# Kernel tuning notes

Measured on AMD Instinct MI355X. Metric: run time of the kernel, lower is better.

## Reference

```python
import jax, jax.numpy as jnp
import numpy as np

N = 100_000   # nodes
E = 6_400_000 # edges
R = 90        # relations
NB = 3        # num_blocks


def setup_inputs() -> dict:
    key = jax.random.key(0)
    ks = jax.random.split(key, 10)
    x = jax.random.normal(ks[0], (N, 3), jnp.float32)
    edge_index = jax.random.randint(ks[1], (2, E), 0, N, dtype=jnp.int32)
    edge_type = jax.random.randint(ks[2], (E,), 0, R, dtype=jnp.int32)
    batch = jnp.zeros((N,), jnp.int32)  # single graph, as in source
    p = lambda k, shape: (jax.random.normal(k, shape, jnp.float32) * 0.1)
    # block-diagonal weights: [R, NB, in_b, out_b]
    W1, root1, b1 = p(ks[3], (R, NB, 1, 2)), p(ks[4], (3, 6)), jnp.zeros((6,), jnp.float32)
    W2, root2, b2 = p(ks[5], (R, NB, 2, 1)), p(ks[6], (6, 3)), jnp.zeros((3,), jnp.float32)
    W3, root3, b3 = p(ks[7], (R, NB, 1, 2)), p(ks[8], (3, 6)), jnp.zeros((6,), jnp.float32)
    return dict(x=x, edge_index=edge_index, batch=batch, edge_type=edge_type,
                W1=W1, root1=root1, b1=b1, W2=W2, root2=root2, b2=b2,
                W3=W3, root3=root3, b3=b3)


def _rgcn(x, src, dst, edge_type, W, root, bias, aggr):
    # block-diagonal per-relation transform of gathered source features
    nb, in_b, out_b = W.shape[1], W.shape[2], W.shape[3]
    xb = x[src].reshape(-1, nb, in_b)                      # [E, NB, in_b]
    msg = jnp.einsum('ebi,ebio->ebo', xb, W[edge_type])    # [E, NB, out_b]
    msg = msg.reshape(-1, nb * out_b)                      # [E, out]
    if aggr == 'mean':
        # per-(dst node, relation) normalization, as in FastRGCNConv
        comb = dst * R + edge_type                         # [E]
        cnt = jax.ops.segment_sum(jnp.ones((msg.shape[0],), msg.dtype), comb,
                                  num_segments=N * R)      # [N*R]
        msg = msg / jnp.clip(cnt[comb], 1.0)[:, None]
    agg = jax.ops.segment_sum(msg, dst, num_segments=N)    # [N, out]
    return agg + x @ root + bias


def reference(x, edge_index, batch, edge_type, W1, root1, b1, W2, root2, b2, W3, root3, b3):
    src, dst = edge_index[0], edge_index[1]
    h = jax.nn.relu(_rgcn(x, src, dst, edge_type, W1, root1, b1, 'mean'))
    # dropout is identity in eval mode
    h = jax.nn.relu(_rgcn(h, src, dst, edge_type, W2, root2, b2, 'add'))
    h = jax.nn.relu(_rgcn(h, src, dst, edge_type, W3, root3, b3, 'mean'))
    # global mean pool over batch (single graph here, kept general)
    num_graphs = 1
    s = jax.ops.segment_sum(h, batch, num_segments=num_graphs)
    c = jax.ops.segment_sum(jnp.ones((h.shape[0],), h.dtype), batch, num_segments=num_graphs)
    pooled = s / jnp.clip(c, 1.0)[:, None]
    return jax.nn.log_softmax(pooled, axis=1)
```

## Files before the change

### kernel.cpp

```cpp
#include <hip/hip_runtime.h>


#define NREL   90
#define BSH    7
#define BNODES 128
#define NBINS  1024
#define NB2    784
#define GCH    8704
#define KPT    17
#define SPK    11056
#define CAPB   10496
#define NV4    6
#define STAGE  9088
#define LPD    16
#define SENT   0xFFFFFFFFu

__device__ __forceinline__ float frelu(float v) { return v > 0.0f ? v : 0.0f; }

__launch_bounds__(512)
__global__ void group_k(const float* __restrict__ x, float4* __restrict__ x4,
                        int N, int gNp,
                        const int* __restrict__ src, const int* __restrict__ dst,
                        const int* __restrict__ et, int* __restrict__ gcount,
                        unsigned* __restrict__ regions, int E) {
    int tid = threadIdx.x;
    if (blockIdx.x < gNp) {
        int i = blockIdx.x * 512 + tid;
        if (i < N) x4[i] = make_float4(x[3 * i], x[3 * i + 1], x[3 * i + 2], 0.0f);
        return;
    }
    __shared__ int s_cur[NB2];
    __shared__ int s_pend[NB2];
    __shared__ int s_off[NB2];
    __shared__ unsigned s_pack[SPK];
    int chunk = blockIdx.x - gNp;
    int e0 = chunk * GCH;
    int cnt = min(GCH, E - e0);
    for (int i = tid; i < NB2; i += 512) s_pend[i] = 0;
    __syncthreads();
    unsigned rec[KPT];
    int bkt[KPT];
#pragma unroll
    for (int k = 0; k < KPT; k++) {
        int q = tid + k * 512;
        if (q < cnt) {
            int e = e0 + q;
            int d = dst[e];
            bkt[k] = d >> BSH;
            rec[k] = (unsigned)src[e] | ((unsigned)et[e] << 17) |
                     ((unsigned)(d & (BNODES - 1)) << 24);
            atomicAdd(&s_pend[bkt[k]], 1);
        } else bkt[k] = -1;
    }
    __syncthreads();
    if (tid < 49) {
        int loc[16];
        int s = 0;
        int b0 = tid * 16;
#pragma unroll
        for (int k = 0; k < 16; k++) {
            int plen = (s_pend[b0 + k] + 3) & ~3;
            loc[k] = plen; s += plen;
        }
        int inc = s;
#pragma unroll
        for (int off = 1; off < 64; off <<= 1) {
            int u = __shfl_up(inc, off);
            if (tid >= off) inc += u;
        }
        int run = inc - s;
#pragma unroll
        for (int k = 0; k < 16; k++) {
            s_cur[b0 + k] = run;
            run += loc[k];
            s_pend[b0 + k] = run;
        }
    }
    __syncthreads();
    int T = s_pend[NB2 - 1];
    for (int b = tid; b < NB2; b += 512) {
        int st = s_cur[b];
        int plen = s_pend[b] - st;
        if (plen > 0) {
            int gb = atomicAdd(&gcount[b], plen);
            if (gb + plen <= CAPB) {
                s_off[b] = gb - st;
            } else {
                s_off[b] = 0x40000000;
                unsigned* reg = regions + (size_t)b * CAPB;
                for (int j = min(gb, CAPB); j < CAPB; j++) reg[j] = SENT;
            }
        } else s_off[b] = 0x40000000;
    }
    for (int i = tid; i < T; i += 512) s_pack[i] = SENT;
    __syncthreads();
#pragma unroll
    for (int k = 0; k < KPT; k++) {
        if (bkt[k] >= 0) {
            int p = atomicAdd(&s_cur[bkt[k]], 1);
            s_pack[p] = rec[k];
        }
    }
    __syncthreads();
    int nv = T >> 2;
    for (int i4 = tid; i4 < nv; i4 += 512) {
        int i = i4 << 2;
        int lo = 0, hi = NB2 - 1;
        while (lo < hi) {
            int mid = (lo + hi) >> 1;
            if (s_pend[mid] > i) hi = mid; else lo = mid + 1;
        }
        int loc = s_off[lo] + i;
        if (loc < CAPB) {
            uint4 v = make_uint4(s_pack[i], s_pack[i + 1],
                                 s_pack[i + 2], s_pack[i + 3]);
            *(uint4*)(regions + (size_t)lo * CAPB + loc) = v;
        }
    }
}

__launch_bounds__(512)
__global__ void sortb_l1_k(const int* __restrict__ gcount, unsigned* regions,
                           int2* __restrict__ rowseg,
                           const float4* __restrict__ x4, const float* __restrict__ W,
                           const float* __restrict__ root, const float* __restrict__ bias,
                           float4* __restrict__ h1p, int N) {
    __shared__ unsigned stage32[STAGE];
    __shared__ unsigned hist8w[BNODES * 90 / 4];
    __shared__ int hh[BNODES], cur[BNODES], base_[BNODES];
    __shared__ float4 w4[NREL * 2];
    int tid = threadIdx.x, b = blockIdx.x;
    for (int i = tid; i < BNODES * 90 / 4; i += 512) hist8w[i] = 0u;
    for (int i = tid; i < NREL * 2; i += 512) {
        int r = i >> 1;
        w4[i] = (i & 1) ? make_float4(W[r * 6 + 4], W[r * 6 + 5], 0.f, 0.f)
                        : make_float4(W[r * 6], W[r * 6 + 1], W[r * 6 + 2], W[r * 6 + 3]);
    }
    __syncthreads();
    int fill = gcount[b];
    if (fill > CAPB) fill = CAPB;
    const uint4* reg4 = (const uint4*)(regions + (size_t)b * CAPB);
    int nv = fill >> 2;
    uint4 rec4[NV4];
#define HIST1(P) if ((P) != SENT) { \
        unsigned bi_ = ((P) >> 24) * 90u + (((P) >> 17) & 127u); \
        atomicAdd(&hist8w[bi_ >> 2], 1u << ((bi_ & 3) << 3)); }
#pragma unroll
    for (int k = 0; k < NV4; k++) {
        int i4 = tid + k * 512;
        if (i4 < nv) {
            uint4 v = reg4[i4];
            rec4[k] = v;
            HIST1(v.x); HIST1(v.y); HIST1(v.z); HIST1(v.w);
        } else {
            rec4[k] = make_uint4(SENT, SENT, SENT, SENT);
        }
    }
    __syncthreads();
    if (tid < BNODES) {
        const unsigned char* h8 = (const unsigned char*)hist8w;
        unsigned s = 0;
        for (int k = 0; k < 90; k++) s += h8[tid * 90 + k];
        hh[tid] = (int)s;
    }
    __syncthreads();
    if (tid < 64) {
        int c0 = hh[2 * tid], c1 = hh[2 * tid + 1];
        int s = c0 + c1;
        int inc = s;
#pragma unroll
        for (int off = 1; off < 64; off <<= 1) {
            int u = __shfl_up(inc, off);
            if (tid >= off) inc += u;
        }
        int run = inc - s;
        base_[2 * tid] = run;          cur[2 * tid] = run;
        base_[2 * tid + 1] = run + c0; cur[2 * tid + 1] = run + c0;
    }
    __syncthreads();
    int cntv = base_[BNODES - 1] + hh[BNODES - 1];
    if (tid < BNODES) {
        int d = (b << BSH) + tid;
        if (d < N) {
            int beg = base_[tid];
            int end = beg + hh[tid];
            if (end > cntv) end = cntv;
            rowseg[d] = make_int2(b * CAPB + beg, b * CAPB + end);
        }
    }
#define PLACE1(P) if ((P) != SENT) { \
        int pos_ = atomicAdd(&cur[(P) >> 24], 1); \
        if (pos_ < STAGE) stage32[pos_] = (P); }
#pragma unroll
    for (int k = 0; k < NV4; k++) {
        PLACE1(rec4[k].x); PLACE1(rec4[k].y); PLACE1(rec4[k].z); PLACE1(rec4[k].w);
    }
    __syncthreads();
    unsigned* regw = regions + (size_t)b * CAPB;
    int grp = tid >> 4, l16 = tid & 15;
#pragma unroll
    for (int rd = 0; rd < 4; rd++) {
        int dL = grp + rd * 32;
        int segb = base_[dL];
        int sege = segb + hh[dL];
        if (sege > cntv) sege = cntv;
        float a0 = 0, a1 = 0, a2 = 0, a3 = 0, a4 = 0, a5 = 0;
        for (int q = segb + l16; q < sege; q += 16) {
            unsigned p = stage32[q];
            unsigned rel = (p >> 17) & 127u;
            unsigned bi = dL * 90u + rel;
            unsigned c = (hist8w[bi >> 2] >> ((bi & 3) << 3)) & 0xFFu;
            regw[q] = (p & 0x00FFFFFFu) | (c << 24);
            float r = __builtin_amdgcn_rcpf((float)c);
            float4 xv = x4[p & 0x1FFFFu];
            unsigned rel2 = rel * 2u;
            float4 wa = w4[rel2], wb = w4[rel2 + 1];
            float x0 = xv.x * r, x1 = xv.y * r, x2 = xv.z * r;
            a0 += x0 * wa.x; a1 += x0 * wa.y;
            a2 += x1 * wa.z; a3 += x1 * wa.w;
            a4 += x2 * wb.x; a5 += x2 * wb.y;
        }
#pragma unroll
        for (int off = 8; off > 0; off >>= 1) {
            a0 += __shfl_down(a0, off); a1 += __shfl_down(a1, off); a2 += __shfl_down(a2, off);
            a3 += __shfl_down(a3, off); a4 += __shfl_down(a4, off); a5 += __shfl_down(a5, off);
        }
        if (l16 == 0) {
            int d = (b << BSH) + dL;
            if (d < N) {
                float4 xv = x4[d];
                float o[6] = {a0, a1, a2, a3, a4, a5};
#pragma unroll
                for (int j = 0; j < 6; j++)
                    o[j] = frelu(o[j] + xv.x * root[j] + xv.y * root[6 + j] +
                                 xv.z * root[12 + j] + bias[j]);
                h1p[d * 2]     = make_float4(o[0], o[1], o[2], o[3]);
                h1p[d * 2 + 1] = make_float4(o[4], o[5], 0.0f, 0.0f);
            }
        }
    }
}

__launch_bounds__(256)
__global__ void l2_g(const int2* __restrict__ rowseg, const unsigned* __restrict__ sorted,
                     const float4* __restrict__ h1p, const float* __restrict__ W,
                     const float* __restrict__ root, const float* __restrict__ bias,
                     float4* __restrict__ h2p, int N) {
    __shared__ float4 w4[NREL * 2];
    for (int i = threadIdx.x; i < NREL * 2; i += 256) {
        int r = i >> 1;
        w4[i] = (i & 1) ? make_float4(W[r * 6 + 4], W[r * 6 + 5], 0.f, 0.f)
                        : make_float4(W[r * 6], W[r * 6 + 1], W[r * 6 + 2], W[r * 6 + 3]);
    }
    __syncthreads();
    int grp = threadIdx.x >> 4, l16 = threadIdx.x & 15;
    int d = blockIdx.x * LPD + grp;
    if (d >= N) return;
    int2 sg = rowseg[d];
    int beg = sg.x, end = sg.y;
    float a0 = 0, a1 = 0, a2 = 0;
    int i = beg + l16;
    for (; i + 48 < end; i += 64) {
        unsigned p[4];
        float4 ha[4], hb[4];
#pragma unroll
        for (int k = 0; k < 4; k++) p[k] = sorted[i + k * 16];
#pragma unroll
        for (int k = 0; k < 4; k++) {
            unsigned s = p[k] & 0x1FFFFu;
            ha[k] = h1p[2 * s]; hb[k] = h1p[2 * s + 1];
        }
#pragma unroll
        for (int k = 0; k < 4; k++) {
            unsigned rel2 = ((p[k] >> 17) & 127u) * 2u;
            float4 wa = w4[rel2], wb = w4[rel2 + 1];
            a0 += ha[k].x * wa.x + ha[k].y * wa.y;
            a1 += ha[k].z * wa.z + ha[k].w * wa.w;
            a2 += hb[k].x * wb.x + hb[k].y * wb.y;
        }
    }
    for (; i < end; i += 16) {
        unsigned p = sorted[i];
        unsigned s = p & 0x1FFFFu;
        float4 ha = h1p[2 * s], hb = h1p[2 * s + 1];
        unsigned rel2 = ((p >> 17) & 127u) * 2u;
        float4 wa = w4[rel2], wb = w4[rel2 + 1];
        a0 += ha.x * wa.x + ha.y * wa.y;
        a1 += ha.z * wa.z + ha.w * wa.w;
        a2 += hb.x * wb.x + hb.y * wb.y;
    }
#pragma unroll
    for (int off = 8; off > 0; off >>= 1) {
        a0 += __shfl_down(a0, off); a1 += __shfl_down(a1, off); a2 += __shfl_down(a2, off);
    }
    if (l16 == 0) {
        float4 ha = h1p[2 * d], hb = h1p[2 * d + 1];
        float hv[6] = {ha.x, ha.y, ha.z, ha.w, hb.x, hb.y};
        float o[3] = {a0, a1, a2};
#pragma unroll
        for (int j = 0; j < 3; j++) {
            float v = o[j] + bias[j];
#pragma unroll
            for (int k = 0; k < 6; k++) v += hv[k] * root[k * 3 + j];
            o[j] = frelu(v);
        }
        h2p[d] = make_float4(o[0], o[1], o[2], 0.0f);
    }
}

__launch_bounds__(256)
__global__ void l3_g(const int2* __restrict__ rowseg, const unsigned* __restrict__ sorted,
                     const float4* __restrict__ h2p, const float* __restrict__ W,
                     const float* __restrict__ root, const float* __restrict__ bias,
                     const int* __restrict__ batch, float* __restrict__ partials, int N) {
    __shared__ float4 w4[NREL * 2];
    __shared__ float redsm[LPD][8];
    for (int i = threadIdx.x; i < NREL * 2; i += 256) {
        int r = i >> 1;
        w4[i] = (i & 1) ? make_float4(W[r * 6 + 4], W[r * 6 + 5], 0.f, 0.f)
                        : make_float4(W[r * 6], W[r * 6 + 1], W[r * 6 + 2], W[r * 6 + 3]);
    }
    __syncthreads();
    int grp = threadIdx.x >> 4, l16 = threadIdx.x & 15;
    int d = blockIdx.x * LPD + grp;
    float a0 = 0, a1 = 0, a2 = 0, a3 = 0, a4 = 0, a5 = 0;
    if (d < N) {
        int2 sg = rowseg[d];
        int beg = sg.x, end = sg.y;
        int i = beg + l16;
        for (; i + 48 < end; i += 64) {
            unsigned p[4];
            float4 xv[4];
#pragma unroll
            for (int k = 0; k < 4; k++) p[k] = sorted[i + k * 16];
#pragma unroll
            for (int k = 0; k < 4; k++) xv[k] = h2p[p[k] & 0x1FFFFu];
#pragma unroll
            for (int k = 0; k < 4; k++) {
                float r = __builtin_amdgcn_rcpf((float)(p[k] >> 24));
                unsigned rel2 = ((p[k] >> 17) & 127u) * 2u;
                float4 wa = w4[rel2], wb = w4[rel2 + 1];
                float x0 = xv[k].x * r, x1 = xv[k].y * r, x2 = xv[k].z * r;
                a0 += x0 * wa.x; a1 += x0 * wa.y;
                a2 += x1 * wa.z; a3 += x1 * wa.w;
                a4 += x2 * wb.x; a5 += x2 * wb.y;
            }
        }
        for (; i < end; i += 16) {
            unsigned p = sorted[i];
            float r = __builtin_amdgcn_rcpf((float)(p >> 24));
            float4 xv = h2p[p & 0x1FFFFu];
            unsigned rel2 = ((p >> 17) & 127u) * 2u;
            float4 wa = w4[rel2], wb = w4[rel2 + 1];
            float x0 = xv.x * r, x1 = xv.y * r, x2 = xv.z * r;
            a0 += x0 * wa.x; a1 += x0 * wa.y;
            a2 += x1 * wa.z; a3 += x1 * wa.w;
            a4 += x2 * wb.x; a5 += x2 * wb.y;
        }
    }
#pragma unroll
    for (int off = 8; off > 0; off >>= 1) {
        a0 += __shfl_down(a0, off); a1 += __shfl_down(a1, off); a2 += __shfl_down(a2, off);
        a3 += __shfl_down(a3, off); a4 += __shfl_down(a4, off); a5 += __shfl_down(a5, off);
    }
    if (l16 == 0) {
        float v[7] = {0, 0, 0, 0, 0, 0, 0};
        if (d < N && batch[d] == 0) {
            float4 xv = h2p[d];
            float o[6] = {a0, a1, a2, a3, a4, a5};
#pragma unroll
            for (int j = 0; j < 6; j++)
                v[j] = frelu(o[j] + xv.x * root[j] + xv.y * root[6 + j] +
                             xv.z * root[12 + j] + bias[j]);
            v[6] = 1.0f;
        }
#pragma unroll
        for (int k = 0; k < 7; k++) redsm[grp][k] = v[k];
    }
    __syncthreads();
    if (threadIdx.x < 7) {
        float t = 0;
#pragma unroll
        for (int g = 0; g < LPD; g++) t += redsm[g][threadIdx.x];
        partials[(size_t)blockIdx.x * 8 + threadIdx.x] = t;
    }
}

__global__ void pool_finalize(const float* __restrict__ partials, int nb,
                              float* __restrict__ out) {
    float v[7] = {0, 0, 0, 0, 0, 0, 0};
    for (int b = threadIdx.x; b < nb; b += blockDim.x) {
#pragma unroll
        for (int k = 0; k < 7; k++) v[k] += partials[(size_t)b * 8 + k];
    }
#pragma unroll
    for (int off = 32; off > 0; off >>= 1) {
#pragma unroll
        for (int k = 0; k < 7; k++) v[k] += __shfl_down(v[k], off);
    }
    __shared__ float sm[16][8];
    int wv = threadIdx.x >> 6, lane = threadIdx.x & 63;
    if (lane == 0) {
#pragma unroll
        for (int k = 0; k < 7; k++) sm[wv][k] = v[k];
    }
    __syncthreads();
    if (threadIdx.x == 0) {
        float t[7] = {0, 0, 0, 0, 0, 0, 0};
        int nw = blockDim.x >> 6;
        for (int q = 0; q < nw; q++) {
#pragma unroll
            for (int k = 0; k < 7; k++) t[k] += sm[q][k];
        }
        float c = t[6] < 1.0f ? 1.0f : t[6];
        float p[6], m = -1e30f;
#pragma unroll
        for (int j = 0; j < 6; j++) { p[j] = t[j] / c; m = fmaxf(m, p[j]); }
        float s = 0.0f;
#pragma unroll
        for (int j = 0; j < 6; j++) s += expf(p[j] - m);
        float lse = m + logf(s);
#pragma unroll
        for (int j = 0; j < 6; j++) out[j] = p[j] - lse;
    }
}

extern "C" void kernel_launch(void* const* d_in, const int* in_sizes, int n_in,
                              void* d_out, int out_size, void* d_ws, size_t ws_size,
                              hipStream_t stream) {
    const float* x     = (const float*)d_in[0];
    const int*   ei    = (const int*)d_in[1];
    const int*   batch = (const int*)d_in[2];
    const int*   etype = (const int*)d_in[3];
    const float* W1    = (const float*)d_in[4];
    const float* root1 = (const float*)d_in[5];
    const float* b1    = (const float*)d_in[6];
    const float* W2    = (const float*)d_in[7];
    const float* root2 = (const float*)d_in[8];
    const float* b2    = (const float*)d_in[9];
    const float* W3    = (const float*)d_in[10];
    const float* root3 = (const float*)d_in[11];
    const float* b3    = (const float*)d_in[12];

    const int N = in_sizes[0] / 3;
    const int E = in_sizes[1] / 2;
    const int* src = ei;
    const int* dst = ei + E;
    const int gG = (E + GCH - 1) / GCH;
    const int NBUCK = (N + BNODES - 1) >> BSH;
    const int gL = (N + LPD - 1) / LPD;

    char* ws = (char*)d_ws;
    size_t off = 0;
    auto alloc = [&](size_t bytes) -> void* {
        void* p = ws + off;
        off += (bytes + 255) & ~(size_t)255;
        return p;
    };
    int*      gcount  = (int*)     alloc(NBINS * sizeof(int));
    size_t zero_bytes = off;
    unsigned* regions = (unsigned*)alloc((size_t)NBUCK * CAPB * sizeof(unsigned));
    int2*     rowseg  = (int2*)    alloc((size_t)N * sizeof(int2));
    float4*   x4      = (float4*)  alloc((size_t)N * sizeof(float4));
    float4*   h1p     = (float4*)  alloc((size_t)N * 2 * sizeof(float4));
    float4*   h2p     = (float4*)  alloc((size_t)N * sizeof(float4));
    float*    partials = (float*)  alloc((size_t)gL * 8 * sizeof(float));

    hipMemsetAsync(d_ws, 0, zero_bytes, stream);

    const int gNp = (N + 511) / 512;

    group_k<<<gNp + gG, 512, 0, stream>>>(x, x4, N, gNp, src, dst, etype,
                                          gcount, regions, E);
    sortb_l1_k<<<NBUCK, 512, 0, stream>>>(gcount, regions, rowseg,
                                          x4, W1, root1, b1, h1p, N);
    l2_g<<<gL, 256, 0, stream>>>(rowseg, regions, h1p, W2, root2, b2, h2p, N);
    l3_g<<<gL, 256, 0, stream>>>(rowseg, regions, h2p, W3, root3, b3, batch, partials, N);
    pool_finalize<<<1, 1024, 0, stream>>>(partials, gL, (float*)d_out);
}
```

Before: 291.2 us.

## Use per-relation prefix counts for placement and split layer-2 gathers across lane pairs

In the layer-1 sort kernel, the packed byte histogram is turned in place into per-(node, relation) exclusive prefix counts. Placement then uses atomics on those prefix bytes, which groups records by relation within each node. This removes the separate per-node sum pass, one barrier and the cur array, and the count is recovered as the difference of adjacent prefix bytes. In layer 2, each pair of lanes splits one edge's two float4 halves of h1p, so each lane issues one float4 gather per edge instead of two, with a smaller unroll. The risks are 8-bit prefix overflow when more than 255 records map to one node, and a branch on comp in the accumulation.

```diff
diff --git a/kernel.cpp b/kernel.cpp
--- a/kernel.cpp
+++ b/kernel.cpp
@@ -127,7 +127,7 @@
                            float4* __restrict__ h1p, int N) {
     __shared__ unsigned stage32[STAGE];
     __shared__ unsigned hist8w[BNODES * 90 / 4];
-    __shared__ int hh[BNODES], cur[BNODES], base_[BNODES];
+    __shared__ int hh[BNODES], base_[BNODES];
     __shared__ float4 w4[NREL * 2];
     int tid = threadIdx.x, b = blockIdx.x;
     for (int i = tid; i < BNODES * 90 / 4; i += 512) hist8w[i] = 0u;
@@ -157,15 +157,25 @@
         }
     }
     __syncthreads();
-    if (tid < BNODES) {
-        const unsigned char* h8 = (const unsigned char*)hist8w;
-        unsigned s = 0;
-        for (int k = 0; k < 90; k++) s += h8[tid * 90 + k];
-        hh[tid] = (int)s;
-    }
-    __syncthreads();
     if (tid < 64) {
-        int c0 = hh[2 * tid], c1 = hh[2 * tid + 1];
+        int wbase = 45 * tid;
+        unsigned run = 0;
+        int hhA = 0;
+#pragma unroll
+        for (int w = 0; w < 45; w++) {
+            unsigned v = hist8w[wbase + w];
+            unsigned nvw = 0;
+#pragma unroll
+            for (int j = 0; j < 4; j++) {
+                if (w * 4 + j == 90) { hhA = (int)run; run = 0; }
+                unsigned c = (v >> (8 * j)) & 0xFFu;
+                nvw |= (run & 0xFFu) << (8 * j);
+                run += c;
+            }
+            hist8w[wbase + w] = nvw;
+        }
+        int c0 = hhA, c1 = (int)run;
+        hh[2 * tid] = c0; hh[2 * tid + 1] = c1;
         int s = c0 + c1;
         int inc = s;
 #pragma unroll
@@ -173,9 +183,9 @@
             int u = __shfl_up(inc, off);
             if (tid >= off) inc += u;
         }
-        int run = inc - s;
-        base_[2 * tid] = run;          cur[2 * tid] = run;
-        base_[2 * tid + 1] = run + c0; cur[2 * tid + 1] = run + c0;
+        int run2 = inc - s;
+        base_[2 * tid] = run2;
+        base_[2 * tid + 1] = run2 + c0;
     }
     __syncthreads();
     int cntv = base_[BNODES - 1] + hh[BNODES - 1];
@@ -189,13 +199,17 @@
         }
     }
 #define PLACE1(P) if ((P) != SENT) { \
-        int pos_ = atomicAdd(&cur[(P) >> 24], 1); \
+        unsigned dL_ = (P) >> 24; \
+        unsigned bi_ = dL_ * 90u + (((P) >> 17) & 127u); \
+        unsigned old_ = atomicAdd(&hist8w[bi_ >> 2], 1u << ((bi_ & 3) << 3)); \
+        int pos_ = base_[dL_] + (int)((old_ >> ((bi_ & 3) << 3)) & 0xFFu); \
         if (pos_ < STAGE) stage32[pos_] = (P); }
 #pragma unroll
     for (int k = 0; k < NV4; k++) {
         PLACE1(rec4[k].x); PLACE1(rec4[k].y); PLACE1(rec4[k].z); PLACE1(rec4[k].w);
     }
     __syncthreads();
+    const unsigned char* h8 = (const unsigned char*)hist8w;
     unsigned* regw = regions + (size_t)b * CAPB;
     int grp = tid >> 4, l16 = tid & 15;
 #pragma unroll
@@ -209,7 +223,7 @@
             unsigned p = stage32[q];
             unsigned rel = (p >> 17) & 127u;
             unsigned bi = dL * 90u + rel;
-            unsigned c = (hist8w[bi >> 2] >> ((bi & 3) << 3)) & 0xFFu;
+            unsigned c = (unsigned)h8[bi] - (rel ? (unsigned)h8[bi - 1] : 0u);
             regw[q] = (p & 0x00FFFFFFu) | (c << 24);
             float r = __builtin_amdgcn_rcpf((float)c);
             float4 xv = x4[p & 0x1FFFFu];
@@ -258,36 +272,29 @@
     if (d >= N) return;
     int2 sg = rowseg[d];
     int beg = sg.x, end = sg.y;
+    int pi = l16 >> 1, comp = l16 & 1;
     float a0 = 0, a1 = 0, a2 = 0;
-    int i = beg + l16;
-    for (; i + 48 < end; i += 64) {
-        unsigned p[4];
-        float4 ha[4], hb[4];
-#pragma unroll
-        for (int k = 0; k < 4; k++) p[k] = sorted[i + k * 16];
-#pragma unroll
-        for (int k = 0; k < 4; k++) {
-            unsigned s = p[k] & 0x1FFFFu;
-            ha[k] = h1p[2 * s]; hb[k] = h1p[2 * s + 1];
-        }
-#pragma unroll
-        for (int k = 0; k < 4; k++) {
-            unsigned rel2 = ((p[k] >> 17) & 127u) * 2u;
-            float4 wa = w4[rel2], wb = w4[rel2 + 1];
-            a0 += ha[k].x * wa.x + ha[k].y * wa.y;
-            a1 += ha[k].z * wa.z + ha[k].w * wa.w;
-            a2 += hb[k].x * wb.x + hb[k].y * wb.y;
-        }
-    }
-    for (; i < end; i += 16) {
+    int i = beg + pi;
+    for (; i + 8 < end; i += 16) {
+        unsigned p0 = sorted[i], p1 = sorted[i + 8];
+        float4 h0 = h1p[(p0 & 0x1FFFFu) * 2u + comp];
+        float4 h1v = h1p[(p1 & 0x1FFFFu) * 2u + comp];
+        float4 w0 = w4[((p0 >> 17) & 127u) * 2u + comp];
+        float4 w1 = w4[((p1 >> 17) & 127u) * 2u + comp];
+        float m00 = h0.x * w0.x + h0.y * w0.y;
+        float m01 = h0.z * w0.z + h0.w * w0.w;
+        float m10 = h1v.x * w1.x + h1v.y * w1.y;
+        float m11 = h1v.z * w1.z + h1v.w * w1.w;
+        if (comp) { a2 += m00 + m10; }
+        else      { a0 += m00 + m10; a1 += m01 + m11; }
+    }
+    for (; i < end; i += 8) {
         unsigned p = sorted[i];
-        unsigned s = p & 0x1FFFFu;
-        float4 ha = h1p[2 * s], hb = h1p[2 * s + 1];
-        unsigned rel2 = ((p >> 17) & 127u) * 2u;
-        float4 wa = w4[rel2], wb = w4[rel2 + 1];
-        a0 += ha.x * wa.x + ha.y * wa.y;
-        a1 += ha.z * wa.z + ha.w * wa.w;
-        a2 += hb.x * wb.x + hb.y * wb.y;
+        float4 h = h1p[(p & 0x1FFFFu) * 2u + comp];
+        float4 w = w4[((p >> 17) & 127u) * 2u + comp];
+        float m0 = h.x * w.x + h.y * w.y;
+        float m1 = h.z * w.z + h.w * w.w;
+        if (comp) a2 += m0; else { a0 += m0; a1 += m1; }
     }
 #pragma unroll
     for (int off = 8; off > 0; off >>= 1) {
```

Result: slower. 304.0 us (+4.4%).

## Replace per-node sorted CSR with bucket-local LDS atomic accumulation across layers

Applied to the files above, without the earlier changes.

Removes the in-block counting sort, staging buffer and rowseg CSR output. All three layers now stream each 128-node bucket's unsorted edge records and accumulate per-destination results with shared-memory float atomics. The per-(node,relation) count histogram is saved to global memory so layer 3 can recompute the mean normalization. This drops the sort's prefix scans, scatter and sorted-record writeback. In exchange, every edge costs several LDS atomic adds, which may contend on hot destinations, and the summation order is no longer deterministic.

```diff
diff --git a/kernel.cpp b/kernel.cpp
--- a/kernel.cpp
+++ b/kernel.cpp
@@ -11,8 +11,7 @@
 #define SPK    11056
 #define CAPB   10496
 #define NV4    6
-#define STAGE  9088
-#define LPD    16
+#define HWORDS (BNODES * NREL / 4)
 #define SENT   0xFFFFFFFFu
 
 __device__ __forceinline__ float frelu(float v) { return v > 0.0f ? v : 0.0f; }
@@ -120,17 +119,18 @@
 }
 
 __launch_bounds__(512)
-__global__ void sortb_l1_k(const int* __restrict__ gcount, unsigned* regions,
-                           int2* __restrict__ rowseg,
+__global__ void sortb_l1_k(const int* __restrict__ gcount,
+                           const unsigned* __restrict__ regions,
+                           unsigned* __restrict__ ghist,
                            const float4* __restrict__ x4, const float* __restrict__ W,
                            const float* __restrict__ root, const float* __restrict__ bias,
                            float4* __restrict__ h1p, int N) {
-    __shared__ unsigned stage32[STAGE];
-    __shared__ unsigned hist8w[BNODES * 90 / 4];
-    __shared__ int hh[BNODES], cur[BNODES], base_[BNODES];
+    __shared__ unsigned hist8w[HWORDS];
     __shared__ float4 w4[NREL * 2];
+    __shared__ float acc[BNODES * 7];
     int tid = threadIdx.x, b = blockIdx.x;
-    for (int i = tid; i < BNODES * 90 / 4; i += 512) hist8w[i] = 0u;
+    for (int i = tid; i < HWORDS; i += 512) hist8w[i] = 0u;
+    for (int i = tid; i < BNODES * 7; i += 512) acc[i] = 0.0f;
     for (int i = tid; i < NREL * 2; i += 512) {
         int r = i >> 1;
         w4[i] = (i & 1) ? make_float4(W[r * 6 + 4], W[r * 6 + 5], 0.f, 0.f)
@@ -142,247 +142,166 @@
     const uint4* reg4 = (const uint4*)(regions + (size_t)b * CAPB);
     int nv = fill >> 2;
     uint4 rec4[NV4];
+#pragma unroll
+    for (int k = 0; k < NV4; k++) {
+        int i4 = tid + k * 512;
+        rec4[k] = (i4 < nv) ? reg4[i4] : make_uint4(SENT, SENT, SENT, SENT);
+    }
 #define HIST1(P) if ((P) != SENT) { \
         unsigned bi_ = ((P) >> 24) * 90u + (((P) >> 17) & 127u); \
         atomicAdd(&hist8w[bi_ >> 2], 1u << ((bi_ & 3) << 3)); }
 #pragma unroll
     for (int k = 0; k < NV4; k++) {
-        int i4 = tid + k * 512;
-        if (i4 < nv) {
-            uint4 v = reg4[i4];
-            rec4[k] = v;
-            HIST1(v.x); HIST1(v.y); HIST1(v.z); HIST1(v.w);
-        } else {
-            rec4[k] = make_uint4(SENT, SENT, SENT, SENT);
-        }
-    }
-    __syncthreads();
-    if (tid < BNODES) {
-        const unsigned char* h8 = (const unsigned char*)hist8w;
-        unsigned s = 0;
-        for (int k = 0; k < 90; k++) s += h8[tid * 90 + k];
-        hh[tid] = (int)s;
-    }
-    __syncthreads();
-    if (tid < 64) {
-        int c0 = hh[2 * tid], c1 = hh[2 * tid + 1];
-        int s = c0 + c1;
-        int inc = s;
-#pragma unroll
-        for (int off = 1; off < 64; off <<= 1) {
-            int u = __shfl_up(inc, off);
-            if (tid >= off) inc += u;
-        }
-        int run = inc - s;
-        base_[2 * tid] = run;          cur[2 * tid] = run;
-        base_[2 * tid + 1] = run + c0; cur[2 * tid + 1] = run + c0;
-    }
-    __syncthreads();
-    int cntv = base_[BNODES - 1] + hh[BNODES - 1];
+        HIST1(rec4[k].x); HIST1(rec4[k].y); HIST1(rec4[k].z); HIST1(rec4[k].w);
+    }
+    __syncthreads();
+    const unsigned char* h8 = (const unsigned char*)hist8w;
+#define L1ACC(P) if ((P) != SENT) { \
+        unsigned dL_ = (P) >> 24, rel_ = ((P) >> 17) & 127u; \
+        float r_ = __builtin_amdgcn_rcpf((float)h8[dL_ * 90 + rel_]); \
+        float4 xv_ = x4[(P) & 0x1FFFFu]; \
+        float4 wa_ = w4[rel_ * 2u], wb_ = w4[rel_ * 2u + 1u]; \
+        float x0_ = xv_.x * r_, x1_ = xv_.y * r_, x2_ = xv_.z * r_; \
+        float* a_ = &acc[dL_ * 7u]; \
+        atomicAdd(a_ + 0, x0_ * wa_.x); atomicAdd(a_ + 1, x0_ * wa_.y); \
+        atomicAdd(a_ + 2, x1_ * wa_.z); atomicAdd(a_ + 3, x1_ * wa_.w); \
+        atomicAdd(a_ + 4, x2_ * wb_.x); atomicAdd(a_ + 5, x2_ * wb_.y); }
+#pragma unroll
+    for (int k = 0; k < NV4; k++) {
+        L1ACC(rec4[k].x); L1ACC(rec4[k].y); L1ACC(rec4[k].z); L1ACC(rec4[k].w);
+    }
+    unsigned* gh = ghist + (size_t)b * HWORDS;
+    for (int i = tid; i < HWORDS; i += 512) gh[i] = hist8w[i];
+    __syncthreads();
     if (tid < BNODES) {
         int d = (b << BSH) + tid;
         if (d < N) {
-            int beg = base_[tid];
-            int end = beg + hh[tid];
-            if (end > cntv) end = cntv;
-            rowseg[d] = make_int2(b * CAPB + beg, b * CAPB + end);
-        }
-    }
-#define PLACE1(P) if ((P) != SENT) { \
-        int pos_ = atomicAdd(&cur[(P) >> 24], 1); \
-        if (pos_ < STAGE) stage32[pos_] = (P); }
-#pragma unroll
-    for (int k = 0; k < NV4; k++) {
-        PLACE1(rec4[k].x); PLACE1(rec4[k].y); PLACE1(rec4[k].z); PLACE1(rec4[k].w);
-    }
-    __syncthreads();
-    unsigned* regw = regions + (size_t)b * CAPB;
-    int grp = tid >> 4, l16 = tid & 15;
-#pragma unroll
-    for (int rd = 0; rd < 4; rd++) {
-        int dL = grp + rd * 32;
-        int segb = base_[dL];
-        int sege = segb + hh[dL];
-        if (sege > cntv) sege = cntv;
-        float a0 = 0, a1 = 0, a2 = 0, a3 = 0, a4 = 0, a5 = 0;
-        for (int q = segb + l16; q < sege; q += 16) {
-            unsigned p = stage32[q];
-            unsigned rel = (p >> 17) & 127u;
-            unsigned bi = dL * 90u + rel;
-            unsigned c = (hist8w[bi >> 2] >> ((bi & 3) << 3)) & 0xFFu;
-            regw[q] = (p & 0x00FFFFFFu) | (c << 24);
-            float r = __builtin_amdgcn_rcpf((float)c);
-            float4 xv = x4[p & 0x1FFFFu];
-            unsigned rel2 = rel * 2u;
-            float4 wa = w4[rel2], wb = w4[rel2 + 1];
-            float x0 = xv.x * r, x1 = xv.y * r, x2 = xv.z * r;
-            a0 += x0 * wa.x; a1 += x0 * wa.y;
-            a2 += x1 * wa.z; a3 += x1 * wa.w;
-            a4 += x2 * wb.x; a5 += x2 * wb.y;
-        }
-#pragma unroll
-        for (int off = 8; off > 0; off >>= 1) {
-            a0 += __shfl_down(a0, off); a1 += __shfl_down(a1, off); a2 += __shfl_down(a2, off);
-            a3 += __shfl_down(a3, off); a4 += __shfl_down(a4, off); a5 += __shfl_down(a5, off);
-        }
-        if (l16 == 0) {
-            int d = (b << BSH) + dL;
-            if (d < N) {
-                float4 xv = x4[d];
-                float o[6] = {a0, a1, a2, a3, a4, a5};
-#pragma unroll
-                for (int j = 0; j < 6; j++)
-                    o[j] = frelu(o[j] + xv.x * root[j] + xv.y * root[6 + j] +
-                                 xv.z * root[12 + j] + bias[j]);
-                h1p[d * 2]     = make_float4(o[0], o[1], o[2], o[3]);
-                h1p[d * 2 + 1] = make_float4(o[4], o[5], 0.0f, 0.0f);
-            }
-        }
-    }
-}
-
-__launch_bounds__(256)
-__global__ void l2_g(const int2* __restrict__ rowseg, const unsigned* __restrict__ sorted,
+            float4 xv = x4[d];
+            float o[6];
+#pragma unroll
+            for (int j = 0; j < 6; j++)
+                o[j] = frelu(acc[tid * 7 + j] + xv.x * root[j] + xv.y * root[6 + j] +
+                             xv.z * root[12 + j] + bias[j]);
+            h1p[d * 2]     = make_float4(o[0], o[1], o[2], o[3]);
+            h1p[d * 2 + 1] = make_float4(o[4], o[5], 0.0f, 0.0f);
+        }
+    }
+}
+
+__launch_bounds__(512)
+__global__ void l2_g(const int* __restrict__ gcount, const unsigned* __restrict__ regions,
                      const float4* __restrict__ h1p, const float* __restrict__ W,
                      const float* __restrict__ root, const float* __restrict__ bias,
                      float4* __restrict__ h2p, int N) {
     __shared__ float4 w4[NREL * 2];
-    for (int i = threadIdx.x; i < NREL * 2; i += 256) {
+    __shared__ float acc[BNODES * 5];
+    int tid = threadIdx.x, b = blockIdx.x;
+    for (int i = tid; i < BNODES * 5; i += 512) acc[i] = 0.0f;
+    for (int i = tid; i < NREL * 2; i += 512) {
         int r = i >> 1;
         w4[i] = (i & 1) ? make_float4(W[r * 6 + 4], W[r * 6 + 5], 0.f, 0.f)
                         : make_float4(W[r * 6], W[r * 6 + 1], W[r * 6 + 2], W[r * 6 + 3]);
     }
     __syncthreads();
-    int grp = threadIdx.x >> 4, l16 = threadIdx.x & 15;
-    int d = blockIdx.x * LPD + grp;
-    if (d >= N) return;
-    int2 sg = rowseg[d];
-    int beg = sg.x, end = sg.y;
-    float a0 = 0, a1 = 0, a2 = 0;
-    int i = beg + l16;
-    for (; i + 48 < end; i += 64) {
-        unsigned p[4];
-        float4 ha[4], hb[4];
-#pragma unroll
-        for (int k = 0; k < 4; k++) p[k] = sorted[i + k * 16];
-#pragma unroll
-        for (int k = 0; k < 4; k++) {
-            unsigned s = p[k] & 0x1FFFFu;
-            ha[k] = h1p[2 * s]; hb[k] = h1p[2 * s + 1];
-        }
-#pragma unroll
-        for (int k = 0; k < 4; k++) {
-            unsigned rel2 = ((p[k] >> 17) & 127u) * 2u;
-            float4 wa = w4[rel2], wb = w4[rel2 + 1];
-            a0 += ha[k].x * wa.x + ha[k].y * wa.y;
-            a1 += ha[k].z * wa.z + ha[k].w * wa.w;
-            a2 += hb[k].x * wb.x + hb[k].y * wb.y;
-        }
-    }
-    for (; i < end; i += 16) {
-        unsigned p = sorted[i];
-        unsigned s = p & 0x1FFFFu;
-        float4 ha = h1p[2 * s], hb = h1p[2 * s + 1];
-        unsigned rel2 = ((p >> 17) & 127u) * 2u;
-        float4 wa = w4[rel2], wb = w4[rel2 + 1];
-        a0 += ha.x * wa.x + ha.y * wa.y;
-        a1 += ha.z * wa.z + ha.w * wa.w;
-        a2 += hb.x * wb.x + hb.y * wb.y;
-    }
-#pragma unroll
-    for (int off = 8; off > 0; off >>= 1) {
-        a0 += __shfl_down(a0, off); a1 += __shfl_down(a1, off); a2 += __shfl_down(a2, off);
-    }
-    if (l16 == 0) {
-        float4 ha = h1p[2 * d], hb = h1p[2 * d + 1];
-        float hv[6] = {ha.x, ha.y, ha.z, ha.w, hb.x, hb.y};
-        float o[3] = {a0, a1, a2};
-#pragma unroll
-        for (int j = 0; j < 3; j++) {
-            float v = o[j] + bias[j];
-#pragma unroll
-            for (int k = 0; k < 6; k++) v += hv[k] * root[k * 3 + j];
-            o[j] = frelu(v);
-        }
-        h2p[d] = make_float4(o[0], o[1], o[2], 0.0f);
-    }
-}
-
-__launch_bounds__(256)
-__global__ void l3_g(const int2* __restrict__ rowseg, const unsigned* __restrict__ sorted,
+    int fill = gcount[b];
+    if (fill > CAPB) fill = CAPB;
+    const uint4* reg4 = (const uint4*)(regions + (size_t)b * CAPB);
+    int nv = fill >> 2;
+#define L2ACC(P) if ((P) != SENT) { \
+        unsigned s_ = (P) & 0x1FFFFu, dL_ = (P) >> 24; \
+        unsigned rel2_ = (((P) >> 17) & 127u) * 2u; \
+        float4 ha_ = h1p[2 * s_], hb_ = h1p[2 * s_ + 1]; \
+        float4 wa_ = w4[rel2_], wb_ = w4[rel2_ + 1]; \
+        float* a_ = &acc[dL_ * 5u]; \
+        atomicAdd(a_ + 0, ha_.x * wa_.x + ha_.y * wa_.y); \
+        atomicAdd(a_ + 1, ha_.z * wa_.z + ha_.w * wa_.w); \
+        atomicAdd(a_ + 2, hb_.x * wb_.x + hb_.y * wb_.y); }
+#pragma unroll
+    for (int k = 0; k < NV4; k++) {
+        int i4 = tid + k * 512;
+        uint4 v = (i4 < nv) ? reg4[i4] : make_uint4(SENT, SENT, SENT, SENT);
+        L2ACC(v.x); L2ACC(v.y); L2ACC(v.z); L2ACC(v.w);
+    }
+    __syncthreads();
+    if (tid < BNODES) {
+        int d = (b << BSH) + tid;
+        if (d < N) {
+            float4 ha = h1p[2 * d], hb = h1p[2 * d + 1];
+            float hv[6] = {ha.x, ha.y, ha.z, ha.w, hb.x, hb.y};
+            float o[3];
+#pragma unroll
+            for (int j = 0; j < 3; j++) {
+                float v = acc[tid * 5 + j] + bias[j];
+#pragma unroll
+                for (int k = 0; k < 6; k++) v += hv[k] * root[k * 3 + j];
+                o[j] = frelu(v);
+            }
+            h2p[d] = make_float4(o[0], o[1], o[2], 0.0f);
+        }
+    }
+}
+
+__launch_bounds__(512)
+__global__ void l3_g(const int* __restrict__ gcount, const unsigned* __restrict__ regions,
+                     const unsigned* __restrict__ ghist,
                      const float4* __restrict__ h2p, const float* __restrict__ W,
                      const float* __restrict__ root, const float* __restrict__ bias,
                      const int* __restrict__ batch, float* __restrict__ partials, int N) {
+    __shared__ unsigned hist8w[HWORDS];
     __shared__ float4 w4[NREL * 2];
-    __shared__ float redsm[LPD][8];
-    for (int i = threadIdx.x; i < NREL * 2; i += 256) {
+    __shared__ float acc[BNODES * 7];
+    __shared__ float redsm[BNODES][8];
+    int tid = threadIdx.x, b = blockIdx.x;
+    const unsigned* gh = ghist + (size_t)b * HWORDS;
+    for (int i = tid; i < HWORDS; i += 512) hist8w[i] = gh[i];
+    for (int i = tid; i < BNODES * 7; i += 512) acc[i] = 0.0f;
+    for (int i = tid; i < NREL * 2; i += 512) {
         int r = i >> 1;
         w4[i] = (i & 1) ? make_float4(W[r * 6 + 4], W[r * 6 + 5], 0.f, 0.f)
                         : make_float4(W[r * 6], W[r * 6 + 1], W[r * 6 + 2], W[r * 6 + 3]);
     }
     __syncthreads();
-    int grp = threadIdx.x >> 4, l16 = threadIdx.x & 15;
-    int d = blockIdx.x * LPD + grp;
-    float a0 = 0, a1 = 0, a2 = 0, a3 = 0, a4 = 0, a5 = 0;
-    if (d < N) {
-        int2 sg = rowseg[d];
-        int beg = sg.x, end = sg.y;
-        int i = beg + l16;
-        for (; i + 48 < end; i += 64) {
-            unsigned p[4];
-            float4 xv[4];
-#pragma unroll
-            for (int k = 0; k < 4; k++) p[k] = sorted[i + k * 16];
-#pragma unroll
-            for (int k = 0; k < 4; k++) xv[k] = h2p[p[k] & 0x1FFFFu];
-#pragma unroll
-            for (int k = 0; k < 4; k++) {
-                float r = __builtin_amdgcn_rcpf((float)(p[k] >> 24));
-                unsigned rel2 = ((p[k] >> 17) & 127u) * 2u;
-                float4 wa = w4[rel2], wb = w4[rel2 + 1];
-                float x0 = xv[k].x * r, x1 = xv[k].y * r, x2 = xv[k].z * r;
-                a0 += x0 * wa.x; a1 += x0 * wa.y;
-                a2 += x1 * wa.z; a3 += x1 * wa.w;
-                a4 += x2 * wb.x; a5 += x2 * wb.y;
-            }
-        }
-        for (; i < end; i += 16) {
-            unsigned p = sorted[i];
-            float r = __builtin_amdgcn_rcpf((float)(p >> 24));
-            float4 xv = h2p[p & 0x1FFFFu];
-            unsigned rel2 = ((p >> 17) & 127u) * 2u;
-            float4 wa = w4[rel2], wb = w4[rel2 + 1];
-            float x0 = xv.x * r, x1 = xv.y * r, x2 = xv.z * r;
-            a0 += x0 * wa.x; a1 += x0 * wa.y;
-            a2 += x1 * wa.z; a3 += x1 * wa.w;
-            a4 += x2 * wb.x; a5 += x2 * wb.y;
-        }
-    }
-#pragma unroll
-    for (int off = 8; off > 0; off >>= 1) {
-        a0 += __shfl_down(a0, off); a1 += __shfl_down(a1, off); a2 += __shfl_down(a2, off);
-        a3 += __shfl_down(a3, off); a4 += __shfl_down(a4, off); a5 += __shfl_down(a5, off);
-    }
-    if (l16 == 0) {
+    int fill = gcount[b];
+    if (fill > CAPB) fill = CAPB;
+    const uint4* reg4 = (const uint4*)(regions + (size_t)b * CAPB);
+    int nv = fill >> 2;
+    const unsigned char* h8 = (const unsigned char*)hist8w;
+#define L3ACC(P) if ((P) != SENT) { \
+        unsigned dL_ = (P) >> 24, rel_ = ((P) >> 17) & 127u; \
+        float r_ = __builtin_amdgcn_rcpf((float)h8[dL_ * 90 + rel_]); \
+        float4 xv_ = h2p[(P) & 0x1FFFFu]; \
+        float4 wa_ = w4[rel_ * 2u], wb_ = w4[rel_ * 2u + 1u]; \
+        float x0_ = xv_.x * r_, x1_ = xv_.y * r_, x2_ = xv_.z * r_; \
+        float* a_ = &acc[dL_ * 7u]; \
+        atomicAdd(a_ + 0, x0_ * wa_.x); atomicAdd(a_ + 1, x0_ * wa_.y); \
+        atomicAdd(a_ + 2, x1_ * wa_.z); atomicAdd(a_ + 3, x1_ * wa_.w); \
+        atomicAdd(a_ + 4, x2_ * wb_.x); atomicAdd(a_ + 5, x2_ * wb_.y); }
+#pragma unroll
+    for (int k = 0; k < NV4; k++) {
+        int i4 = tid + k * 512;
+        uint4 v = (i4 < nv) ? reg4[i4] : make_uint4(SENT, SENT, SENT, SENT);
+        L3ACC(v.x); L3ACC(v.y); L3ACC(v.z); L3ACC(v.w);
+    }
+    __syncthreads();
+    if (tid < BNODES) {
+        int d = (b << BSH) + tid;
         float v[7] = {0, 0, 0, 0, 0, 0, 0};
         if (d < N && batch[d] == 0) {
             float4 xv = h2p[d];
-            float o[6] = {a0, a1, a2, a3, a4, a5};
 #pragma unroll
             for (int j = 0; j < 6; j++)
-                v[j] = frelu(o[j] + xv.x * root[j] + xv.y * root[6 + j] +
+                v[j] = frelu(acc[tid * 7 + j] + xv.x * root[j] + xv.y * root[6 + j] +
                              xv.z * root[12 + j] + bias[j]);
             v[6] = 1.0f;
         }
 #pragma unroll
-        for (int k = 0; k < 7; k++) redsm[grp][k] = v[k];
-    }
-    __syncthreads();
-    if (threadIdx.x < 7) {
+        for (int k = 0; k < 7; k++) redsm[tid][k] = v[k];
+    }
+    __syncthreads();
+    if (tid < 7) {
         float t = 0;
-#pragma unroll
-        for (int g = 0; g < LPD; g++) t += redsm[g][threadIdx.x];
-        partials[(size_t)blockIdx.x * 8 + threadIdx.x] = t;
+        for (int g = 0; g < BNODES; g++) t += redsm[g][tid];
+        partials[(size_t)b * 8 + tid] = t;
     }
 }
 
@@ -448,7 +367,6 @@
     const int* dst = ei + E;
     const int gG = (E + GCH - 1) / GCH;
     const int NBUCK = (N + BNODES - 1) >> BSH;
-    const int gL = (N + LPD - 1) / LPD;
 
     char* ws = (char*)d_ws;
     size_t off = 0;
@@ -460,11 +378,11 @@
     int*      gcount  = (int*)     alloc(NBINS * sizeof(int));
     size_t zero_bytes = off;
     unsigned* regions = (unsigned*)alloc((size_t)NBUCK * CAPB * sizeof(unsigned));
-    int2*     rowseg  = (int2*)    alloc((size_t)N * sizeof(int2));
+    unsigned* ghist   = (unsigned*)alloc((size_t)NBUCK * HWORDS * sizeof(unsigned));
     float4*   x4      = (float4*)  alloc((size_t)N * sizeof(float4));
     float4*   h1p     = (float4*)  alloc((size_t)N * 2 * sizeof(float4));
     float4*   h2p     = (float4*)  alloc((size_t)N * sizeof(float4));
-    float*    partials = (float*)  alloc((size_t)gL * 8 * sizeof(float));
+    float*    partials = (float*)  alloc((size_t)NBUCK * 8 * sizeof(float));
 
     hipMemsetAsync(d_ws, 0, zero_bytes, stream);
 
@@ -472,9 +390,10 @@
 
     group_k<<<gNp + gG, 512, 0, stream>>>(x, x4, N, gNp, src, dst, etype,
                                           gcount, regions, E);
-    sortb_l1_k<<<NBUCK, 512, 0, stream>>>(gcount, regions, rowseg,
+    sortb_l1_k<<<NBUCK, 512, 0, stream>>>(gcount, regions, ghist,
                                           x4, W1, root1, b1, h1p, N);
-    l2_g<<<gL, 256, 0, stream>>>(rowseg, regions, h1p, W2, root2, b2, h2p, N);
-    l3_g<<<gL, 256, 0, stream>>>(rowseg, regions, h2p, W3, root3, b3, batch, partials, N);
-    pool_finalize<<<1, 1024, 0, stream>>>(partials, gL, (float*)d_out);
-}
+    l2_g<<<NBUCK, 512, 0, stream>>>(gcount, regions, h1p, W2, root2, b2, h2p, N);
+    l3_g<<<NBUCK, 512, 0, stream>>>(gcount, regions, ghist, h2p, W3, root3, b3,
+                                    batch, partials, N);
+    pool_finalize<<<1, 1024, 0, stream>>>(partials, NBUCK, (float*)d_out);
+}
```

Result: slower. 820.6 us (+181.8%).
